# Kernel optimization log

Measured on AMD Instinct MI355X. Metric: run time of the kernel, lower is better.

Reference implementation:

```python
import jax, jax.numpy as jnp
import numpy as np

N, E = 100000, 640000
IN_DIM, OUT_DIM, MSG_DIM, TIME_DIM, HEADS = 128, 128, 128, 128, 2
C = OUT_DIM // HEADS  # per-head channels = 64
EDGE_DIM = MSG_DIM + TIME_DIM  # 256


def setup_inputs() -> dict:
    key = jax.random.key(0)
    ks = jax.random.split(key, 16)
    s = 0.05
    return {
        "x": jax.random.normal(ks[0], (N, IN_DIM), jnp.float32),
        "last_update": jax.random.uniform(ks[1], (N,), jnp.float32, 0.0, 100.0),
        "t": jax.random.uniform(ks[2], (E,), jnp.float32, 100.0, 200.0),
        "msg": jax.random.normal(ks[3], (E, MSG_DIM), jnp.float32),
        "time_w": jax.random.normal(ks[4], (TIME_DIM,), jnp.float32) * s,
        "time_b": jax.random.normal(ks[5], (TIME_DIM,), jnp.float32) * s,
        "Wq": jax.random.normal(ks[6], (IN_DIM, HEADS * C), jnp.float32) * s,
        "bq": jnp.zeros((HEADS * C,), jnp.float32),
        "Wk": jax.random.normal(ks[7], (IN_DIM, HEADS * C), jnp.float32) * s,
        "bk": jnp.zeros((HEADS * C,), jnp.float32),
        "Wv": jax.random.normal(ks[8], (IN_DIM, HEADS * C), jnp.float32) * s,
        "bv": jnp.zeros((HEADS * C,), jnp.float32),
        "We": jax.random.normal(ks[9], (EDGE_DIM, HEADS * C), jnp.float32) * s,
        "Wskip": jax.random.normal(ks[10], (IN_DIM, HEADS * C), jnp.float32) * s,
        "bskip": jnp.zeros((HEADS * C,), jnp.float32),
        "edge_index": jax.random.randint(ks[11], (2, E), 0, N, jnp.int64),
    }


def reference(x, last_update, t, msg, time_w, time_b, Wq, bq, Wk, bk, Wv, bv,
              We, Wskip, bskip, edge_index):
    src = edge_index[0]  # source node j per edge
    dst = edge_index[1]  # target node i per edge

    # Time encoding: phi(dt) = cos(w*dt + b)
    rel_t = t - last_update[src]                      # [E]
    rel_t_enc = jnp.cos(rel_t[:, None] * time_w[None, :] + time_b)  # [E, TIME_DIM]
    edge_attr = jnp.concatenate([rel_t_enc, msg], axis=-1)           # [E, EDGE_DIM]

    # Node-level projections (dense GEMMs), then edge gathers
    q_n = x @ Wq + bq   # [N, H*C]
    k_n = x @ Wk + bk
    v_n = x @ Wv + bv
    e_proj = (edge_attr @ We).reshape(E, HEADS, C)    # [E, H, C]

    q = q_n[dst].reshape(E, HEADS, C)
    k = k_n[src].reshape(E, HEADS, C) + e_proj
    v = v_n[src].reshape(E, HEADS, C) + e_proj

    # Per-edge attention logits, scatter-softmax over incoming edges of each dst
    alpha = jnp.sum(q * k, axis=-1) / jnp.sqrt(jnp.float32(C))  # [E, H]
    a_max = jax.ops.segment_max(alpha, dst, num_segments=N)      # [N, H]
    a_max = jnp.where(jnp.isfinite(a_max), a_max, 0.0)
    a_exp = jnp.exp(alpha - a_max[dst])                          # [E, H]
    a_sum = jax.ops.segment_sum(a_exp, dst, num_segments=N)      # [N, H]
    attn = a_exp / (a_sum[dst] + 1e-16)                          # [E, H]

    # Weighted aggregate + skip connection (concat heads)
    out = jax.ops.segment_sum(attn[..., None] * v, dst, num_segments=N)  # [N, H, C]
    out = out.reshape(N, HEADS * C) + (x @ Wskip + bskip)
    return out
```

## Files before the change

kernel.cpp:

```cpp
#include <hip/hip_runtime.h>
#include <hip/hip_bf16.h>

#define NN 100000
#define EE 640000
#define NB_SCAN 98
#define NTILE 10000
#define G_EDGE 1024

typedef short bf16x8 __attribute__((ext_vector_type(8)));
typedef float f32x4 __attribute__((ext_vector_type(4)));

__device__ __forceinline__ ushort f2bf(float f){
  uint u = __float_as_uint(f);
  u += 0x7fffu + ((u >> 16) & 1u);
  return (ushort)(u >> 16);
}
__device__ __forceinline__ float bf2f(ushort s){ return __uint_as_float(((uint)s) << 16); }
__device__ __forceinline__ uint pack2(float a, float b){ return ((uint)f2bf(b) << 16) | (uint)f2bf(a); }
__device__ __forceinline__ uint swz(uint row, uint colB, uint strideB){
  return row * strideB + (colB ^ ((row & 7u) << 4));
}

__global__ void k_prep(const float* __restrict__ Wq, const float* __restrict__ Wk,
                       const float* __restrict__ Wv, const float* __restrict__ Wsk,
                       const float* __restrict__ We,
                       ushort* __restrict__ W4t, ushort* __restrict__ Wet,
                       int* __restrict__ deg){
  int tid = blockIdx.x * 256 + threadIdx.x;
  if (tid < 512 * 128){
    int col = tid >> 7, k = tid & 127;
    const float* W = (col < 128) ? Wq : ((col < 256) ? Wk : ((col < 384) ? Wv : Wsk));
    W4t[tid] = f2bf(W[k * 128 + (col & 127)]);
  }
  if (tid < 128 * 256){
    int col = tid >> 8, k = tid & 255;
    Wet[tid] = f2bf(We[k * 128 + col]);
  }
  if (tid < NN) deg[tid] = 0;
}

__global__ __launch_bounds__(256) void k_node(
    const float* __restrict__ x, const ushort* __restrict__ W4t,
    const float* __restrict__ bq, const float* __restrict__ bk,
    const float* __restrict__ bv, const float* __restrict__ bsk,
    ushort* __restrict__ q_n, ushort* __restrict__ kv,
    float* __restrict__ out){
  __shared__ ushort As[64 * 128];
  __shared__ ushort Bs[128 * 128];
  char* Ab = (char*)As; char* Bb = (char*)Bs;
  int tid = threadIdx.x;
  int n0 = blockIdx.x * 64;
  {
    int row = tid >> 2, part = tid & 3;
    int gr = n0 + row;
    for (int j = 0; j < 4; j++){
      float4 a = make_float4(0.f,0.f,0.f,0.f), b = a;
      if (gr < NN){
        const float4* p = (const float4*)(x + (size_t)gr * 128 + part * 32 + j * 8);
        a = p[0]; b = p[1];
      }
      uint4 w; w.x = pack2(a.x,a.y); w.y = pack2(a.z,a.w); w.z = pack2(b.x,b.y); w.w = pack2(b.z,b.w);
      *(uint4*)(Ab + swz(row, (uint)(part * 64 + j * 16), 256)) = w;
    }
  }
  int wid = tid >> 6, l = tid & 63, lr = l & 15, lg = l >> 4;
  for (int chunk = 0; chunk < 4; ++chunk){
    if (chunk) __syncthreads();
    {
      int row = tid >> 1, half = tid & 1;
      const ushort* src = W4t + (size_t)(chunk * 128 + row) * 128 + half * 64;
      for (int j = 0; j < 8; j++){
        uint4 w = *(const uint4*)(src + j * 8);
        *(uint4*)(Bb + swz(row, (uint)(half * 128 + j * 16), 256)) = w;
      }
    }
    __syncthreads();
    f32x4 acc[8];
    for (int i = 0; i < 8; i++) acc[i] = (f32x4){0.f,0.f,0.f,0.f};
    for (int ks = 0; ks < 4; ++ks){
      bf16x8 a = *(bf16x8*)(Ab + swz(wid * 16 + lr, (uint)(ks * 64 + lg * 16), 256));
      for (int cf = 0; cf < 8; ++cf){
        bf16x8 b = *(bf16x8*)(Bb + swz(cf * 16 + lr, (uint)(ks * 64 + lg * 16), 256));
        acc[cf] = __builtin_amdgcn_mfma_f32_16x16x32_bf16(a, b, acc[cf], 0, 0, 0);
      }
    }
    for (int cf = 0; cf < 8; ++cf){
      for (int i = 0; i < 4; i++){
        int row = wid * 16 + lg * 4 + i;
        int gr = n0 + row;
        if (gr >= NN) continue;
        int col = cf * 16 + lr;
        float v = acc[cf][i];
        if (chunk == 0)      q_n[(size_t)gr * 128 + col] = f2bf(v + bq[col]);
        else if (chunk == 1) kv[(size_t)gr * 256 + ((col >> 1) << 2) + (col & 1)]     = f2bf(v + bk[col]);
        else if (chunk == 2) kv[(size_t)gr * 256 + ((col >> 1) << 2) + 2 + (col & 1)] = f2bf(v + bv[col]);
        else                 out[(size_t)gr * 128 + col] = v + bsk[col];
      }
    }
  }
}

__global__ __launch_bounds__(512, 2) void k_edge2(
    const float* __restrict__ tt, const float* __restrict__ lu,
    const float* __restrict__ msg, const float* __restrict__ tw,
    const float* __restrict__ tb, const int* __restrict__ ei,
    const ushort* __restrict__ Wet, ushort* __restrict__ ep){
  __shared__ ushort A[3][64][256];
  char* Ab = (char*)A;
  int tid = threadIdx.x;
  int wid = tid >> 6, l = tid & 63, lr = l & 15, lg = l >> 4;
  int rg = wid >> 1, cg = wid & 1;
  bf16x8 Bf[4][8];
  {
    const char* WB = (const char*)Wet;
    #pragma unroll
    for (int cf = 0; cf < 4; ++cf){
      #pragma unroll
      for (int ks = 0; ks < 8; ++ks)
        Bf[cf][ks] = *(const bf16x8*)(WB + (size_t)(cg*64 + cf*16 + lr)*512 + ks*64 + lg*16);
    }
  }
  int nT = (NTILE - (int)blockIdx.x + G_EDGE - 1) / G_EDGE;
  bool isMsg = (wid < 4);
  int er = (tid & 255) >> 2, qq = tid & 3;
  float4 mreg[8];
  float tvW = 0.f, luW = 0.f, tvN = 0.f;
  int eiN = 0;
  f32x4 acc[4];
  #pragma unroll
  for (int cf = 0; cf < 4; ++cf) acc[cf] = (f32x4){0.f,0.f,0.f,0.f};

  {
    int e = (int)blockIdx.x * 64 + er;
    if (isMsg){
      const float4* p = (const float4*)(msg + (size_t)e * 128 + qq * 32);
      #pragma unroll
      for (int j = 0; j < 8; ++j) mreg[j] = p[j];
    } else {
      tvN = tt[e]; eiN = ei[e];
      luW = lu[eiN];
      tvW = tvN;
    }
  }

  for (int i = 0; i <= nT; ++i){
    if (i < nT){
      char* dst = Ab + (i % 3) * 32768;
      if (isMsg){
        #pragma unroll
        for (int j = 0; j < 4; ++j){
          float4 a = mreg[2*j], b = mreg[2*j+1];
          uint4 w; w.x = pack2(a.x,a.y); w.y = pack2(a.z,a.w); w.z = pack2(b.x,b.y); w.w = pack2(b.z,b.w);
          *(uint4*)(dst + er*512 + ((uint)(256 + qq*64 + j*16) ^ ((uint)(er&7)<<4))) = w;
        }
      } else {
        float rel = tvW - luW;
        #pragma unroll
        for (int j = 0; j < 4; ++j){
          int k0 = qq*32 + j*8;
          float4 wa = *(const float4*)(tw + k0), wb = *(const float4*)(tw + k0 + 4);
          float4 ba = *(const float4*)(tb + k0), bb = *(const float4*)(tb + k0 + 4);
          float c0 = __cosf(fmaf(rel, wa.x, ba.x));
          float c1 = __cosf(fmaf(rel, wa.y, ba.y));
          float c2 = __cosf(fmaf(rel, wa.z, ba.z));
          float c3 = __cosf(fmaf(rel, wa.w, ba.w));
          float c4 = __cosf(fmaf(rel, wb.x, bb.x));
          float c5 = __cosf(fmaf(rel, wb.y, bb.y));
          float c6 = __cosf(fmaf(rel, wb.z, bb.z));
          float c7 = __cosf(fmaf(rel, wb.w, bb.w));
          uint4 w; w.x = pack2(c0,c1); w.y = pack2(c2,c3); w.z = pack2(c4,c5); w.w = pack2(c6,c7);
          *(uint4*)(dst + er*512 + ((uint)(qq*64 + j*16) ^ ((uint)(er&7)<<4))) = w;
        }
      }
      if (i + 1 < nT){
        int e = ((int)blockIdx.x + (i+1) * G_EDGE) * 64 + er;
        if (isMsg){
          const float4* p = (const float4*)(msg + (size_t)e * 128 + qq * 32);
          #pragma unroll
          for (int j = 0; j < 8; ++j) mreg[j] = p[j];
        } else {
          tvN = tt[e]; eiN = ei[e];
        }
      }
      __builtin_amdgcn_sched_barrier(0);
      asm volatile("s_waitcnt lgkmcnt(0)" ::: "memory");
      __builtin_amdgcn_s_barrier();
      __builtin_amdgcn_sched_barrier(0);
    }
    if (i > 0){
      char* src = Ab + ((i - 1) % 3) * 32768;
      #pragma unroll
      for (int ks = 0; ks < 8; ++ks){
        bf16x8 a = *(bf16x8*)(src + (rg*16+lr)*512 + (((uint)(ks*64 + lg*16)) ^ ((uint)(lr&7)<<4)));
        #pragma unroll
        for (int cf = 0; cf < 4; ++cf)
          acc[cf] = __builtin_amdgcn_mfma_f32_16x16x32_bf16(a, Bf[cf][ks], acc[cf], 0, 0, 0);
      }
      if (!isMsg && i + 1 < nT){ luW = lu[eiN]; tvW = tvN; }
      int e0s = ((int)blockIdx.x + (i-1) * G_EDGE) * 64;
      #pragma unroll
      for (int cf = 0; cf < 4; ++cf){
        #pragma unroll
        for (int i2 = 0; i2 < 4; ++i2){
          int row = rg*16 + lg*4 + i2, col = cg*64 + cf*16 + lr;
          ep[(size_t)(e0s + row)*128 + col] = f2bf(acc[cf][i2]);
        }
        acc[cf] = (f32x4){0.f,0.f,0.f,0.f};
      }
    } else {
      if (!isMsg && i + 1 < nT){ luW = lu[eiN]; tvW = tvN; }
    }
  }
}

__global__ void k_hist(const int* __restrict__ ei, int* __restrict__ deg){
  int e = blockIdx.x * 256 + threadIdx.x;
  if (e < EE) atomicAdd(&deg[ei[EE + e]], 1);
}

__global__ __launch_bounds__(256) void k_scan1(const int* __restrict__ deg,
                                               int* __restrict__ start,
                                               int* __restrict__ partial){
  __shared__ int sums[256];
  int b = blockIdx.x, tid = threadIdx.x;
  int base = b * 1024 + tid * 4;
  int d0 = (base + 0 < NN) ? deg[base + 0] : 0;
  int d1 = (base + 1 < NN) ? deg[base + 1] : 0;
  int d2 = (base + 2 < NN) ? deg[base + 2] : 0;
  int d3 = (base + 3 < NN) ? deg[base + 3] : 0;
  int s = d0 + d1 + d2 + d3;
  sums[tid] = s;
  __syncthreads();
  for (int off = 1; off < 256; off <<= 1){
    int v = (tid >= off) ? sums[tid - off] : 0;
    __syncthreads();
    sums[tid] += v;
    __syncthreads();
  }
  int excl = sums[tid] - s;
  if (base + 0 < NN) start[base + 0] = excl;
  if (base + 1 < NN) start[base + 1] = excl + d0;
  if (base + 2 < NN) start[base + 2] = excl + d0 + d1;
  if (base + 3 < NN) start[base + 3] = excl + d0 + d1 + d2;
  if (tid == 255) partial[b] = sums[255];
}

__global__ void k_scan2(int* __restrict__ partial){
  if (threadIdx.x == 0){
    int run = 0;
    for (int b = 0; b < NB_SCAN; b++){ int t = partial[b]; partial[b] = run; run += t; }
  }
}

__global__ void k_scan3(int* __restrict__ start, const int* __restrict__ partial,
                        int* __restrict__ cursor){
  int i = blockIdx.x * 256 + threadIdx.x;
  if (i < NN){
    int v = start[i] + partial[i >> 10];
    start[i] = v;
    cursor[i] = v;
  }
  if (i == 0) start[NN] = EE;
}

__global__ void k_place(const int* __restrict__ ei, int* __restrict__ cursor,
                        uint2* __restrict__ sorted2){
  int e = blockIdx.x * 256 + threadIdx.x;
  if (e < EE){
    int dst = ei[EE + e];
    int src = ei[e];
    int pos = atomicAdd(&cursor[dst], 1);
    sorted2[pos] = make_uint2((uint)e, (uint)src);
  }
}

__global__ __launch_bounds__(256) void k_gather(
    const ushort* __restrict__ q_n, const ushort* __restrict__ kv,
    const ushort* __restrict__ ep, const int* __restrict__ start,
    const uint2* __restrict__ sorted2, float* __restrict__ out){
  int wave = (blockIdx.x * 256 + threadIdx.x) >> 6;
  if (wave >= NN) return;
  int n = wave;
  int l = threadIdx.x & 63;
  int c = l * 2;
  int s0 = start[n], s1 = start[n + 1];
  uint qq = *(const uint*)(q_n + (size_t)n * 128 + c);
  float q0 = bf2f(qq & 0xffff), q1 = bf2f(qq >> 16);
  float acc0 = 0.f, acc1 = 0.f, denom = 0.f;
  int i = s0;
  for (; i + 2 <= s1; i += 2){
    uint2 p0 = sorted2[i], p1 = sorted2[i + 1];
    uint2 kv0 = *(const uint2*)(kv + (size_t)p0.y * 256 + c * 2);
    uint2 kv1 = *(const uint2*)(kv + (size_t)p1.y * 256 + c * 2);
    uint e0 = *(const uint*)(ep + (size_t)p0.x * 128 + c);
    uint e1 = *(const uint*)(ep + (size_t)p1.x * 128 + c);
    float pa0 = bf2f(e0 & 0xffff), pa1 = bf2f(e0 >> 16);
    float pb0 = bf2f(e1 & 0xffff), pb1 = bf2f(e1 >> 16);
    float ka = q0 * (bf2f(kv0.x & 0xffff) + pa0) + q1 * (bf2f(kv0.x >> 16) + pa1);
    float kb = q0 * (bf2f(kv1.x & 0xffff) + pb0) + q1 * (bf2f(kv1.x >> 16) + pb1);
    #pragma unroll
    for (int off = 16; off > 0; off >>= 1){
      ka += __shfl_xor(ka, off);
      kb += __shfl_xor(kb, off);
    }
    float ea = __expf(ka * 0.125f), eb = __expf(kb * 0.125f);
    denom += ea + eb;
    acc0 += ea * (bf2f(kv0.y & 0xffff) + pa0) + eb * (bf2f(kv1.y & 0xffff) + pb0);
    acc1 += ea * (bf2f(kv0.y >> 16) + pa1) + eb * (bf2f(kv1.y >> 16) + pb1);
  }
  if (i < s1){
    uint2 p0 = sorted2[i];
    uint2 kv0 = *(const uint2*)(kv + (size_t)p0.y * 256 + c * 2);
    uint e0 = *(const uint*)(ep + (size_t)p0.x * 128 + c);
    float pa0 = bf2f(e0 & 0xffff), pa1 = bf2f(e0 >> 16);
    float ka = q0 * (bf2f(kv0.x & 0xffff) + pa0) + q1 * (bf2f(kv0.x >> 16) + pa1);
    #pragma unroll
    for (int off = 16; off > 0; off >>= 1) ka += __shfl_xor(ka, off);
    float ea = __expf(ka * 0.125f);
    denom += ea;
    acc0 += ea * (bf2f(kv0.y & 0xffff) + pa0);
    acc1 += ea * (bf2f(kv0.y >> 16) + pa1);
  }
  float inv = 1.0f / (denom + 1e-16f);
  size_t o = (size_t)n * 128 + c;
  out[o]     += acc0 * inv;
  out[o + 1] += acc1 * inv;
}

extern "C" void kernel_launch(void* const* d_in, const int* in_sizes, int n_in,
                              void* d_out, int out_size, void* d_ws, size_t ws_size,
                              hipStream_t stream) {
  const float* x   = (const float*)d_in[0];
  const float* lu  = (const float*)d_in[1];
  const float* t   = (const float*)d_in[2];
  const float* msg = (const float*)d_in[3];
  const float* tw  = (const float*)d_in[4];
  const float* tb  = (const float*)d_in[5];
  const float* Wq  = (const float*)d_in[6];
  const float* bq  = (const float*)d_in[7];
  const float* Wk  = (const float*)d_in[8];
  const float* bk  = (const float*)d_in[9];
  const float* Wv  = (const float*)d_in[10];
  const float* bv  = (const float*)d_in[11];
  const float* We  = (const float*)d_in[12];
  const float* Wsk = (const float*)d_in[13];
  const float* bsk = (const float*)d_in[14];
  const int*   ei  = (const int*)d_in[15];
  float* out = (float*)d_out;

  char* w = (char*)d_ws;
  size_t off = 0;
  auto nxt = [&](size_t b){ size_t r = off; off += (b + 255) & ~(size_t)255; return r; };
  ushort* q_n   = (ushort*)(w + nxt((size_t)NN * 128 * 2));
  ushort* kv    = (ushort*)(w + nxt((size_t)NN * 256 * 2));
  ushort* epj   = (ushort*)(w + nxt((size_t)EE * 128 * 2));
  ushort* W4t   = (ushort*)(w + nxt((size_t)512 * 128 * 2));
  ushort* Wet   = (ushort*)(w + nxt((size_t)128 * 256 * 2));
  int* deg      = (int*)(w + nxt((size_t)NN * 4));
  int* start    = (int*)(w + nxt((size_t)(NN + 1) * 4));
  int* cursor   = (int*)(w + nxt((size_t)NN * 4));
  int* partial  = (int*)(w + nxt((size_t)(NB_SCAN + 1) * 4));
  uint2* sorted2 = (uint2*)(w + nxt((size_t)EE * 8));

  k_prep<<<(NN + 255) / 256, 256, 0, stream>>>(Wq, Wk, Wv, Wsk, We, W4t, Wet, deg);
  k_node<<<(NN + 63) / 64, 256, 0, stream>>>(x, W4t, bq, bk, bv, bsk, q_n, kv, out);
  k_edge2<<<G_EDGE, 512, 0, stream>>>(t, lu, msg, tw, tb, ei, Wet, epj);
  k_hist<<<(EE + 255) / 256, 256, 0, stream>>>(ei, deg);
  k_scan1<<<NB_SCAN, 256, 0, stream>>>(deg, start, partial);
  k_scan2<<<1, 64, 0, stream>>>(partial);
  k_scan3<<<(NN + 255) / 256, 256, 0, stream>>>(start, partial, cursor);
  k_place<<<(EE + 255) / 256, 256, 0, stream>>>(ei, cursor, sorted2);
  k_gather<<<(NN * 64 + 255) / 256, 256, 0, stream>>>(q_n, kv, epj, start, sorted2, out);
}
```

Baseline: 508.9 us.

## Rewrite edge projection as LDS-free register MFMA with precomputed relative times

```diff
diff --git a/kernel.cpp b/kernel.cpp
--- a/kernel.cpp
+++ b/kernel.cpp
@@ -4,8 +4,7 @@
 #define NN 100000
 #define EE 640000
 #define NB_SCAN 98
-#define NTILE 10000
-#define G_EDGE 1024
+#define G_E3 2048
 
 typedef short bf16x8 __attribute__((ext_vector_type(8)));
 typedef float f32x4 __attribute__((ext_vector_type(4)));
@@ -100,115 +99,73 @@
   }
 }
 
-__global__ __launch_bounds__(512, 2) void k_edge2(
-    const float* __restrict__ tt, const float* __restrict__ lu,
-    const float* __restrict__ msg, const float* __restrict__ tw,
-    const float* __restrict__ tb, const int* __restrict__ ei,
+__global__ void k_rel(const float* __restrict__ tt, const float* __restrict__ lu,
+                      const int* __restrict__ ei, float* __restrict__ rel){
+  int e = blockIdx.x * 256 + threadIdx.x;
+  if (e < EE) rel[e] = tt[e] - lu[ei[e]];
+}
+
+__global__ __launch_bounds__(256, 2) void k_edge3(
+    const float* __restrict__ rel, const float* __restrict__ msg,
+    const float* __restrict__ tw, const float* __restrict__ tb,
     const ushort* __restrict__ Wet, ushort* __restrict__ ep){
-  __shared__ ushort A[3][64][256];
-  char* Ab = (char*)A;
   int tid = threadIdx.x;
   int wid = tid >> 6, l = tid & 63, lr = l & 15, lg = l >> 4;
-  int rg = wid >> 1, cg = wid & 1;
-  bf16x8 Bf[4][8];
-  {
-    const char* WB = (const char*)Wet;
-    #pragma unroll
-    for (int cf = 0; cf < 4; ++cf){
+  int gw = (int)blockIdx.x * 4 + wid;
+  int half = gw & 1;
+  bf16x8 Af[4][8];
+  const char* WB = (const char*)Wet;
+  #pragma unroll
+  for (int rt = 0; rt < 4; ++rt)
+    #pragma unroll
+    for (int ks = 0; ks < 8; ++ks)
+      Af[rt][ks] = *(const bf16x8*)(WB + (size_t)(half*64 + rt*16 + lr)*512 + ks*64 + lg*16);
+
+  for (int g = gw >> 1; g < EE/16; g += G_E3 * 2){
+    int e0 = g * 16;
+    float4 m[8];
+    const float* MB = msg + (size_t)(e0 + lr) * 128 + lg * 8;
+    #pragma unroll
+    for (int ks = 0; ks < 4; ++ks){
+      m[2*ks]   = *(const float4*)(MB + ks * 32);
+      m[2*ks+1] = *(const float4*)(MB + ks * 32 + 4);
+    }
+    float relv = rel[e0 + lr];
+    bf16x8 B[8];
+    #pragma unroll
+    for (int ks = 0; ks < 4; ++ks){
+      int k0 = ks * 32 + lg * 8;
+      float4 wa = *(const float4*)(tw + k0), wb = *(const float4*)(tw + k0 + 4);
+      float4 ba = *(const float4*)(tb + k0), bb = *(const float4*)(tb + k0 + 4);
+      float c0 = __cosf(fmaf(relv, wa.x, ba.x));
+      float c1 = __cosf(fmaf(relv, wa.y, ba.y));
+      float c2 = __cosf(fmaf(relv, wa.z, ba.z));
+      float c3 = __cosf(fmaf(relv, wa.w, ba.w));
+      float c4 = __cosf(fmaf(relv, wb.x, bb.x));
+      float c5 = __cosf(fmaf(relv, wb.y, bb.y));
+      float c6 = __cosf(fmaf(relv, wb.z, bb.z));
+      float c7 = __cosf(fmaf(relv, wb.w, bb.w));
+      uint4 w; w.x = pack2(c0,c1); w.y = pack2(c2,c3); w.z = pack2(c4,c5); w.w = pack2(c6,c7);
+      B[ks] = *(bf16x8*)&w;
+    }
+    #pragma unroll
+    for (int ks = 0; ks < 4; ++ks){
+      float4 a = m[2*ks], b = m[2*ks+1];
+      uint4 w; w.x = pack2(a.x,a.y); w.y = pack2(a.z,a.w); w.z = pack2(b.x,b.y); w.w = pack2(b.z,b.w);
+      B[4+ks] = *(bf16x8*)&w;
+    }
+    f32x4 acc[4];
+    #pragma unroll
+    for (int rt = 0; rt < 4; ++rt) acc[rt] = (f32x4){0.f,0.f,0.f,0.f};
+    #pragma unroll
+    for (int ks = 0; ks < 8; ++ks)
       #pragma unroll
-      for (int ks = 0; ks < 8; ++ks)
-        Bf[cf][ks] = *(const bf16x8*)(WB + (size_t)(cg*64 + cf*16 + lr)*512 + ks*64 + lg*16);
-    }
-  }
-  int nT = (NTILE - (int)blockIdx.x + G_EDGE - 1) / G_EDGE;
-  bool isMsg = (wid < 4);
-  int er = (tid & 255) >> 2, qq = tid & 3;
-  float4 mreg[8];
-  float tvW = 0.f, luW = 0.f, tvN = 0.f;
-  int eiN = 0;
-  f32x4 acc[4];
-  #pragma unroll
-  for (int cf = 0; cf < 4; ++cf) acc[cf] = (f32x4){0.f,0.f,0.f,0.f};
-
-  {
-    int e = (int)blockIdx.x * 64 + er;
-    if (isMsg){
-      const float4* p = (const float4*)(msg + (size_t)e * 128 + qq * 32);
-      #pragma unroll
-      for (int j = 0; j < 8; ++j) mreg[j] = p[j];
-    } else {
-      tvN = tt[e]; eiN = ei[e];
-      luW = lu[eiN];
-      tvW = tvN;
-    }
-  }
-
-  for (int i = 0; i <= nT; ++i){
-    if (i < nT){
-      char* dst = Ab + (i % 3) * 32768;
-      if (isMsg){
-        #pragma unroll
-        for (int j = 0; j < 4; ++j){
-          float4 a = mreg[2*j], b = mreg[2*j+1];
-          uint4 w; w.x = pack2(a.x,a.y); w.y = pack2(a.z,a.w); w.z = pack2(b.x,b.y); w.w = pack2(b.z,b.w);
-          *(uint4*)(dst + er*512 + ((uint)(256 + qq*64 + j*16) ^ ((uint)(er&7)<<4))) = w;
-        }
-      } else {
-        float rel = tvW - luW;
-        #pragma unroll
-        for (int j = 0; j < 4; ++j){
-          int k0 = qq*32 + j*8;
-          float4 wa = *(const float4*)(tw + k0), wb = *(const float4*)(tw + k0 + 4);
-          float4 ba = *(const float4*)(tb + k0), bb = *(const float4*)(tb + k0 + 4);
-          float c0 = __cosf(fmaf(rel, wa.x, ba.x));
-          float c1 = __cosf(fmaf(rel, wa.y, ba.y));
-          float c2 = __cosf(fmaf(rel, wa.z, ba.z));
-          float c3 = __cosf(fmaf(rel, wa.w, ba.w));
-          float c4 = __cosf(fmaf(rel, wb.x, bb.x));
-          float c5 = __cosf(fmaf(rel, wb.y, bb.y));
-          float c6 = __cosf(fmaf(rel, wb.z, bb.z));
-          float c7 = __cosf(fmaf(rel, wb.w, bb.w));
-          uint4 w; w.x = pack2(c0,c1); w.y = pack2(c2,c3); w.z = pack2(c4,c5); w.w = pack2(c6,c7);
-          *(uint4*)(dst + er*512 + ((uint)(qq*64 + j*16) ^ ((uint)(er&7)<<4))) = w;
-        }
-      }
-      if (i + 1 < nT){
-        int e = ((int)blockIdx.x + (i+1) * G_EDGE) * 64 + er;
-        if (isMsg){
-          const float4* p = (const float4*)(msg + (size_t)e * 128 + qq * 32);
-          #pragma unroll
-          for (int j = 0; j < 8; ++j) mreg[j] = p[j];
-        } else {
-          tvN = tt[e]; eiN = ei[e];
-        }
-      }
-      __builtin_amdgcn_sched_barrier(0);
-      asm volatile("s_waitcnt lgkmcnt(0)" ::: "memory");
-      __builtin_amdgcn_s_barrier();
-      __builtin_amdgcn_sched_barrier(0);
-    }
-    if (i > 0){
-      char* src = Ab + ((i - 1) % 3) * 32768;
-      #pragma unroll
-      for (int ks = 0; ks < 8; ++ks){
-        bf16x8 a = *(bf16x8*)(src + (rg*16+lr)*512 + (((uint)(ks*64 + lg*16)) ^ ((uint)(lr&7)<<4)));
-        #pragma unroll
-        for (int cf = 0; cf < 4; ++cf)
-          acc[cf] = __builtin_amdgcn_mfma_f32_16x16x32_bf16(a, Bf[cf][ks], acc[cf], 0, 0, 0);
-      }
-      if (!isMsg && i + 1 < nT){ luW = lu[eiN]; tvW = tvN; }
-      int e0s = ((int)blockIdx.x + (i-1) * G_EDGE) * 64;
-      #pragma unroll
-      for (int cf = 0; cf < 4; ++cf){
-        #pragma unroll
-        for (int i2 = 0; i2 < 4; ++i2){
-          int row = rg*16 + lg*4 + i2, col = cg*64 + cf*16 + lr;
-          ep[(size_t)(e0s + row)*128 + col] = f2bf(acc[cf][i2]);
-        }
-        acc[cf] = (f32x4){0.f,0.f,0.f,0.f};
-      }
-    } else {
-      if (!isMsg && i + 1 < nT){ luW = lu[eiN]; tvW = tvN; }
+      for (int rt = 0; rt < 4; ++rt)
+        acc[rt] = __builtin_amdgcn_mfma_f32_16x16x32_bf16(Af[rt][ks], B[ks], acc[rt], 0, 0, 0);
+    #pragma unroll
+    for (int rt = 0; rt < 4; ++rt){
+      uint2 w = make_uint2(pack2(acc[rt][0], acc[rt][1]), pack2(acc[rt][2], acc[rt][3]));
+      *(uint2*)(ep + (size_t)(e0 + lr) * 128 + half * 64 + rt * 16 + lg * 4) = w;
     }
   }
 }
@@ -361,10 +318,12 @@
   int* cursor   = (int*)(w + nxt((size_t)NN * 4));
   int* partial  = (int*)(w + nxt((size_t)(NB_SCAN + 1) * 4));
   uint2* sorted2 = (uint2*)(w + nxt((size_t)EE * 8));
+  float* rel    = (float*)(w + nxt((size_t)EE * 4));
 
   k_prep<<<(NN + 255) / 256, 256, 0, stream>>>(Wq, Wk, Wv, Wsk, We, W4t, Wet, deg);
   k_node<<<(NN + 63) / 64, 256, 0, stream>>>(x, W4t, bq, bk, bv, bsk, q_n, kv, out);
-  k_edge2<<<G_EDGE, 512, 0, stream>>>(t, lu, msg, tw, tb, ei, Wet, epj);
+  k_rel<<<(EE + 255) / 256, 256, 0, stream>>>(t, lu, ei, rel);
+  k_edge3<<<G_E3, 256, 0, stream>>>(rel, msg, tw, tb, Wet, epj);
   k_hist<<<(EE + 255) / 256, 256, 0, stream>>>(ei, deg);
   k_scan1<<<NB_SCAN, 256, 0, stream>>>(deg, start, partial);
   k_scan2<<<1, 64, 0, stream>>>(partial);
```

New measurement: 479.7 us. -5.7%, faster.
